# Kernel tuning notes

Hardware: AMD Instinct MI355X
Metric: run time of the kernel (lower is better)

## Reference

```python
import jax, jax.numpy as jnp
import numpy as np


def setup_inputs() -> dict:
    key = jax.random.key(0)
    B, N = 128, 512
    SSMap = jax.random.normal(key, (B, N, N), dtype=jnp.float32)
    return {"SSMap": SSMap}


def reference(SSMap):
    # SSMap: [B, N, N]. For each superdiagonal offset d = 1..N-2 (length L = N-d,
    # the final length-1 diagonal is excluded), compute unbiased std of
    # (diag * L / 5) = std(diag) * L / 5, then mean over diagonals per batch item.
    B, N, _ = SSMap.shape
    K = N - 2  # number of diagonals used (offsets 1..N-2)
    P = N - 1  # max diagonal length
    k = jnp.arange(K)[:, None]            # diagonal index -> offset d = k+1
    p = jnp.arange(P)[None, :]            # position along diagonal
    rows = jnp.broadcast_to(p, (K, P))    # row index i = p
    cols = p + k + 1                      # col index j = p + d
    mask = cols < N                       # valid positions: p < N - d
    cols = jnp.minimum(cols, N - 1)
    diags = SSMap[:, rows, cols]          # [B, K, P] padded diagonals
    maskf = mask.astype(SSMap.dtype)      # [K, P]
    lens = jnp.sum(maskf, axis=1)         # [K], L = N - 1 - k (>= 2)
    mean = jnp.sum(diags * maskf, axis=2) / lens            # [B, K]
    dev = (diags - mean[:, :, None]) * maskf                # masked deviations
    var = jnp.sum(dev * dev, axis=2) / (lens - 1.0)         # unbiased (ddof=1)
    scaled = jnp.sqrt(var) * lens / 5.0                     # std(diag * L / 5)
    loss = jnp.mean(scaled, axis=1)                         # [B]
    return (loss, jax.lax.stop_gradient(loss))
```

## Files before the change

### kernel.cpp

```cpp
#include <hip/hip_runtime.h>
#include <math.h>

constexpr int B_ = 128;
constexpr int N_ = 512;
constexpr int K_ = 510;
constexpr int SPLIT = 16;

__global__ __launch_bounds__(256) void diag_partial_kernel(
    const float* __restrict__ in, float* __restrict__ ws) {
  const int b = blockIdx.x / SPLIT;
  const int s = blockIdx.x % SPLIT;
  const int t = threadIdx.x;
  const float* base = in + (size_t)b * N_ * N_;
  const int la = (N_ - 1) - t;
  const int lb = t;
  constexpr size_t step = (size_t)SPLIT * (N_ + 1);
  const float* pa = base + (size_t)s * (N_ + 1) + 1 + t;
  const float* pb = base + (size_t)s * (N_ + 1) + (N_ - t);
  float Sa0 = 0.f, Qa0 = 0.f, Sa1 = 0.f, Qa1 = 0.f;
  float Sb0 = 0.f, Qb0 = 0.f, Sb1 = 0.f, Qb1 = 0.f;
  int p = s;
  for (; p + 3 * SPLIT < la; p += 4 * SPLIT) {
    float a0 = pa[0];
    float a1 = pa[step];
    float a2 = pa[2 * step];
    float a3 = pa[3 * step];
    float b0 = 0.f, b1 = 0.f, b2 = 0.f, b3 = 0.f;
    if (p < lb)             b0 = pb[0];
    if (p + SPLIT < lb)     b1 = pb[step];
    if (p + 2 * SPLIT < lb) b2 = pb[2 * step];
    if (p + 3 * SPLIT < lb) b3 = pb[3 * step];
    Sa0 += a0; Qa0 = fmaf(a0, a0, Qa0);
    Sa1 += a1; Qa1 = fmaf(a1, a1, Qa1);
    Sa0 += a2; Qa0 = fmaf(a2, a2, Qa0);
    Sa1 += a3; Qa1 = fmaf(a3, a3, Qa1);
    Sb0 += b0; Qb0 = fmaf(b0, b0, Qb0);
    Sb1 += b1; Qb1 = fmaf(b1, b1, Qb1);
    Sb0 += b2; Qb0 = fmaf(b2, b2, Qb0);
    Sb1 += b3; Qb1 = fmaf(b3, b3, Qb1);
    pa += 4 * step;
    pb += 4 * step;
  }
  for (; p < la; p += SPLIT) {
    float a0 = pa[0];
    Sa0 += a0; Qa0 = fmaf(a0, a0, Qa0);
    if (p < lb) {
      float b0 = pb[0];
      Sb0 += b0; Qb0 = fmaf(b0, b0, Qb0);
    }
    pa += step;
    pb += step;
  }
  float* w = ws + (size_t)blockIdx.x * (2 * N_);
  w[t] = Sa0 + Sa1;
  w[t + N_] = Qa0 + Qa1;
  w[(N_ - 1) - t] = Sb0 + Sb1;
  w[(N_ - 1) - t + N_] = Qb0 + Qb1;
}

__global__ __launch_bounds__(512) void finalize_kernel(
    const float* __restrict__ ws, float* __restrict__ out) {
  __shared__ float red[8];
  const int b = blockIdx.x;
  const int t = threadIdx.x;
  float Ssum = 0.0f, Qsum = 0.0f;
#pragma unroll
  for (int s = 0; s < SPLIT; ++s) {
    const float* w = ws + (size_t)(b * SPLIT + s) * (2 * N_);
    Ssum += w[t];
    Qsum += w[t + N_];
  }
  float scaled = 0.0f;
  if (t < K_) {
    float len = (float)(N_ - 1 - t);
    float mean = Ssum / len;
    float var = (Qsum - Ssum * mean) / (len - 1.0f);
    var = fmaxf(var, 0.0f);
    scaled = sqrtf(var) * len * 0.2f;
  }
  for (int off = 32; off > 0; off >>= 1)
    scaled += __shfl_down(scaled, off, 64);
  const int wid = t >> 6;
  if ((t & 63) == 0) red[wid] = scaled;
  __syncthreads();
  if (t == 0) {
    float tot = 0.0f;
    for (int i = 0; i < 8; ++i) tot += red[i];
    float loss = tot / (float)K_;
    out[b] = loss;
    out[B_ + b] = loss;
  }
}

extern "C" void kernel_launch(void* const* d_in, const int* in_sizes, int n_in,
                              void* d_out, int out_size, void* d_ws, size_t ws_size,
                              hipStream_t stream) {
  const float* in = (const float*)d_in[0];
  float* out = (float*)d_out;
  float* ws = (float*)d_ws;
  diag_partial_kernel<<<B_ * SPLIT, 256, 0, stream>>>(in, ws);
  finalize_kernel<<<B_, 512, 0, stream>>>(ws, out);
}
```

Measured before the change: 179.5 us.

## Assign contiguous row bands per block instead of strided diagonal positions

Each block now walks two contiguous 16-row bands of the matrix, rows 16s..16s+15 for both diagonals and a mirrored band near the bottom for the long diagonal only. Previously it visited every 16th row. The fixed trip count allows full unrolling with no runtime loop, and keeps each block's accesses in nearby rows, which should improve cache-line reuse between adjacent diagonal elements. The cost is predicated loads in the lower band and a correctness dependence on SPLIT=16 with N=512 so that the two bands tile all rows.

```diff
diff --git a/kernel.cpp b/kernel.cpp
--- a/kernel.cpp
+++ b/kernel.cpp
@@ -14,43 +14,44 @@
   const float* base = in + (size_t)b * N_ * N_;
   const int la = (N_ - 1) - t;
   const int lb = t;
-  constexpr size_t step = (size_t)SPLIT * (N_ + 1);
-  const float* pa = base + (size_t)s * (N_ + 1) + 1 + t;
-  const float* pb = base + (size_t)s * (N_ + 1) + (N_ - t);
   float Sa0 = 0.f, Qa0 = 0.f, Sa1 = 0.f, Qa1 = 0.f;
   float Sb0 = 0.f, Qb0 = 0.f, Sb1 = 0.f, Qb1 = 0.f;
-  int p = s;
-  for (; p + 3 * SPLIT < la; p += 4 * SPLIT) {
-    float a0 = pa[0];
-    float a1 = pa[step];
-    float a2 = pa[2 * step];
-    float a3 = pa[3 * step];
-    float b0 = 0.f, b1 = 0.f, b2 = 0.f, b3 = 0.f;
-    if (p < lb)             b0 = pb[0];
-    if (p + SPLIT < lb)     b1 = pb[step];
-    if (p + 2 * SPLIT < lb) b2 = pb[2 * step];
-    if (p + 3 * SPLIT < lb) b3 = pb[3 * step];
-    Sa0 += a0; Qa0 = fmaf(a0, a0, Qa0);
-    Sa1 += a1; Qa1 = fmaf(a1, a1, Qa1);
-    Sa0 += a2; Qa0 = fmaf(a2, a2, Qa0);
-    Sa1 += a3; Qa1 = fmaf(a3, a3, Qa1);
-    Sb0 += b0; Qb0 = fmaf(b0, b0, Qb0);
-    Sb1 += b1; Qb1 = fmaf(b1, b1, Qb1);
-    Sb0 += b2; Qb0 = fmaf(b2, b2, Qb0);
-    Sb1 += b3; Qb1 = fmaf(b3, b3, Qb1);
-    pa += 4 * step;
-    pb += 4 * step;
+
+  {
+    const int r0 = 16 * s;
+    const float* pa = base + (size_t)r0 * (N_ + 1) + 1 + t;
+    const float* pb = base + (size_t)r0 * (N_ + 1) + (N_ - t);
+#pragma unroll
+    for (int i = 0; i < 16; i += 2) {
+      const int p0 = r0 + i;
+      const int p1 = r0 + i + 1;
+      float a0 = pa[0];
+      float a1 = pa[N_ + 1];
+      float b0 = (p0 < lb) ? pb[0] : 0.f;
+      float b1 = (p1 < lb) ? pb[N_ + 1] : 0.f;
+      Sa0 += a0; Qa0 = fmaf(a0, a0, Qa0);
+      Sa1 += a1; Qa1 = fmaf(a1, a1, Qa1);
+      Sb0 += b0; Qb0 = fmaf(b0, b0, Qb0);
+      Sb1 += b1; Qb1 = fmaf(b1, b1, Qb1);
+      pa += 2 * (N_ + 1);
+      pb += 2 * (N_ + 1);
+    }
   }
-  for (; p < la; p += SPLIT) {
-    float a0 = pa[0];
-    Sa0 += a0; Qa0 = fmaf(a0, a0, Qa0);
-    if (p < lb) {
-      float b0 = pb[0];
-      Sb0 += b0; Qb0 = fmaf(b0, b0, Qb0);
+  {
+    const int r0 = (N_ - 16) - 16 * s;
+    const float* pa = base + (size_t)r0 * (N_ + 1) + 1 + t;
+#pragma unroll
+    for (int i = 0; i < 16; i += 2) {
+      const int p0 = r0 + i;
+      const int p1 = r0 + i + 1;
+      float a0 = (p0 < la) ? pa[0] : 0.f;
+      float a1 = (p1 < la) ? pa[N_ + 1] : 0.f;
+      Sa0 += a0; Qa0 = fmaf(a0, a0, Qa0);
+      Sa1 += a1; Qa1 = fmaf(a1, a1, Qa1);
+      pa += 2 * (N_ + 1);
     }
-    pa += step;
-    pb += step;
   }
+
   float* w = ws + (size_t)blockIdx.x * (2 * N_);
   w[t] = Sa0 + Sa1;
   w[t + N_] = Qa0 + Qa1;
```

Result: slower. 184.6 us (+2.9%).
